# Kernel tuning notes

Measured on AMD Instinct MI355X. Metric: run time of the kernel, lower is better.

## Reference

```python
import jax, jax.numpy as jnp
import numpy as np
import math

B, S, D, H = 2, 2048, 2048, 16
DH = D // H  # 128


def _rope(x, cos, sin):
    # x: [b, s, h, dh]; cos/sin: [s, dh//2]
    b, s, h, dh = x.shape
    x2 = x.reshape(b, s, h, dh // 2, 2)
    a, bb = x2[..., 0], x2[..., 1]
    c = cos[None, :, None, :]
    sn = sin[None, :, None, :]
    out = jnp.stack([a * c - bb * sn, a * sn + bb * c], axis=-1)
    return out.reshape(b, s, h, dh)


def setup_inputs() -> dict:
    key = jax.random.key(0)
    ks = jax.random.split(key, 6)
    x = jax.random.normal(ks[0], (B, S, D), dtype=jnp.float32)
    # RoPE frequencies (theta=10000) as cos/sin of shape [S, DH//2]
    inv_freq = 1.0 / (10000.0 ** (np.arange(0, DH, 2, dtype=np.float32) / DH))
    t = np.arange(S, dtype=np.float32)
    ang = jnp.asarray(np.outer(t, inv_freq))  # [S, DH//2]
    freqs_cos = jnp.cos(ang)
    freqs_sin = jnp.sin(ang)
    # causal additive mask [1,1,S,S]
    neg = jnp.finfo(jnp.float32).min
    mask = jnp.where(jnp.tril(jnp.ones((S, S), dtype=bool)), 0.0, neg)[None, None]
    sc = 0.02
    wq = jax.random.normal(ks[1], (D, D), dtype=jnp.float32) * sc
    wk = jax.random.normal(ks[2], (D, D), dtype=jnp.float32) * sc
    wv = jax.random.normal(ks[3], (D, D), dtype=jnp.float32) * sc
    wo = jax.random.normal(ks[4], (D, D), dtype=jnp.float32) * sc
    return {"x": x, "freqs_cos": freqs_cos, "freqs_sin": freqs_sin,
            "mask": mask, "wq": wq, "wk": wk, "wv": wv, "wo": wo}


def reference(x, freqs_cos, freqs_sin, mask, wq, wk, wv, wo):
    b, s, _ = x.shape
    # torch Linear: y = x @ W.T (weights stored [out, in])
    xq = (x @ wq.T).reshape(b, s, H, DH)
    xk = (x @ wk.T).reshape(b, s, H, DH)
    xv = (x @ wv.T).reshape(b, s, H, DH)
    xq = _rope(xq, freqs_cos, freqs_sin)
    xk = _rope(xk, freqs_cos, freqs_sin)
    # [b, h, s, dh]
    q = xq.transpose(0, 2, 1, 3)
    k = xk.transpose(0, 2, 1, 3)
    v = xv.transpose(0, 2, 1, 3)
    scores = jnp.einsum('bhqd,bhkd->bhqk', q, k) / math.sqrt(DH)
    scores = scores + mask
    attn = jax.nn.softmax(scores, axis=-1)  # dropout p=0 (eval)
    out = jnp.einsum('bhqk,bhkd->bhqd', attn, v)
    out = out.transpose(0, 2, 1, 3).reshape(b, s, D)
    return out @ wo.T
```

## Files before the change

### kernel.cpp

```cpp
#include <hip/hip_runtime.h>

#define B_ 2
#define S_ 2048
#define D_ 2048
#define H_ 16
#define DH_ 128

typedef __bf16 bf16_8 __attribute__((ext_vector_type(8)));
typedef __bf16 bf16_4 __attribute__((ext_vector_type(4)));
typedef float f32x4 __attribute__((ext_vector_type(4)));

__device__ __forceinline__ f32x4 mfma16(bf16_8 a, bf16_8 b, f32x4 c) {
  return __builtin_amdgcn_mfma_f32_16x16x32_bf16(a, b, c, 0, 0, 0);
}

__device__ __forceinline__ bf16_8 load8(const float* p) {
  f32x4 a = *(const f32x4*)p;
  f32x4 b = *(const f32x4*)(p + 4);
  bf16_8 r;
  r[0] = (__bf16)a[0]; r[1] = (__bf16)a[1]; r[2] = (__bf16)a[2]; r[3] = (__bf16)a[3];
  r[4] = (__bf16)b[0]; r[5] = (__bf16)b[1]; r[6] = (__bf16)b[2]; r[7] = (__bf16)b[3];
  return r;
}

__device__ __forceinline__ void async16(const __bf16* g, __bf16* l) {
  __builtin_amdgcn_global_load_lds(
      (const __attribute__((address_space(1))) void*)g,
      (__attribute__((address_space(3))) void*)l, 16, 0, 0);
}

__global__ __launch_bounds__(256) void cvt_all(
    const float* __restrict__ x, const float* __restrict__ wq,
    const float* __restrict__ wk, const float* __restrict__ wv,
    const float* __restrict__ wo, __bf16* __restrict__ xb,
    __bf16* __restrict__ wqb, __bf16* __restrict__ wkb,
    __bf16* __restrict__ wvb, __bf16* __restrict__ wob)
{
  const int W8 = (D_ * D_) / 8;
  int i = blockIdx.x * 256 + threadIdx.x;
  if (i < 2 * W8) {
    *(bf16_8*)(xb + (size_t)i * 8) = load8(x + (size_t)i * 8);
  } else {
    int j = i - 2 * W8;
    int sel = j >> 19, off = j & (W8 - 1);
    const float* s = sel == 0 ? wq : sel == 1 ? wk : sel == 2 ? wv : wo;
    __bf16* d = sel == 0 ? wqb : sel == 1 ? wkb : sel == 2 ? wvb : wob;
    *(bf16_8*)(d + (size_t)off * 8) = load8(s + (size_t)off * 8);
  }
}

template <bool WB>
__global__ __launch_bounds__(256) void qkv_gemm(
    const __bf16* __restrict__ A,
    const float* __restrict__ wqf, const float* __restrict__ wkf,
    const float* __restrict__ wvf,
    const __bf16* __restrict__ wqb, const __bf16* __restrict__ wkb,
    const __bf16* __restrict__ wvb,
    const float* __restrict__ fc, const float* __restrict__ fs,
    __bf16* __restrict__ Qo, __bf16* __restrict__ Ko, __bf16* __restrict__ Vo)
{
  constexpr int TILE = 128 * 32;
  constexpr int STAGE_ELEMS = WB ? 4 * TILE : (128 * 32 + 128 * 40);
  constexpr int TS_ELEMS = 64 * 136;
  constexpr int SM_ELEMS = STAGE_ELEMS > TS_ELEMS ? STAGE_ELEMS : TS_ELEMS;
  __shared__ __align__(16) __bf16 smem[SM_ELEMS];

  const int tid = threadIdx.x;
  const int wave = tid >> 6, lane = tid & 63;
  const int quad = lane >> 4, l16 = lane & 15;
  const int m0 = blockIdx.y * 128, n0 = blockIdx.x * 128;
  const int wsel = n0 >> 11, nloc = n0 & 2047;
  const int wm = (wave >> 1) * 64, wn = (wave & 1) * 64;
  const __bf16* agl = A + (size_t)(m0 + wave * 32 + (lane >> 2)) * 2048 + (lane & 3) * 8;
  f32x4 acc[4][4] = {};
  if (WB) {
    const __bf16* Wb = wsel == 0 ? wqb : wsel == 1 ? wkb : wvb;
    const __bf16* wgl = Wb + (size_t)(nloc + wave * 32 + (lane >> 2)) * 2048 + (lane & 3) * 8;
    auto STAGE = [&](int k0, int p) {
      __bf16* ab = smem + p * TILE + (wave * 32) * 32;
      __bf16* wb2 = smem + 2 * TILE + p * TILE + (wave * 32) * 32;
      async16(agl + k0,             ab);
      async16(agl + 16 * 2048 + k0, ab + 16 * 32);
      async16(wgl + k0,             wb2);
      async16(wgl + 16 * 2048 + k0, wb2 + 16 * 32);
    };
    STAGE(0, 0);
#pragma unroll 2
    for (int it = 0; it < 64; ++it) {
      const int p = it & 1;
      if (it + 1 < 64) {
        STAGE((it + 1) * 32, p ^ 1);
        asm volatile("s_waitcnt vmcnt(4)" ::: "memory");
      } else {
        asm volatile("s_waitcnt vmcnt(0)" ::: "memory");
      }
      __builtin_amdgcn_s_barrier();
      asm volatile("" ::: "memory");
      const __bf16* Ab = smem + p * TILE;
      const __bf16* Wbuf = smem + 2 * TILE + p * TILE;
      bf16_8 af[4], bfr[4];
      for (int i = 0; i < 4; ++i) {
        af[i]  = *(const bf16_8*)(Ab   + (wm + i * 16 + l16) * 32 + quad * 8);
        bfr[i] = *(const bf16_8*)(Wbuf + (wn + i * 16 + l16) * 32 + quad * 8);
      }
      for (int mi = 0; mi < 4; ++mi)
        for (int ni = 0; ni < 4; ++ni)
          acc[mi][ni] = mfma16(af[mi], bfr[ni], acc[mi][ni]);
      asm volatile("s_waitcnt lgkmcnt(0)" ::: "memory");
      __builtin_amdgcn_s_barrier();
      asm volatile("" ::: "memory");
    }
  } else {
    auto As = (__bf16(*)[32])smem;
    auto Ws = (__bf16(*)[40])(smem + 128 * 32);
    const float* W = wsel == 0 ? wqf : wsel == 1 ? wkf : wvf;
    const int srow = tid >> 1, scol = (tid & 1) * 16;
    const float* wg = W + (size_t)(nloc + srow) * 2048 + scol;
    for (int k0 = 0; k0 < 2048; k0 += 32) {
      __syncthreads();
      async16(agl + k0,             &As[wave * 32][0]);
      async16(agl + 16 * 2048 + k0, &As[wave * 32 + 16][0]);
      *(bf16_8*)&Ws[srow][scol]     = load8(wg + k0);
      *(bf16_8*)&Ws[srow][scol + 8] = load8(wg + k0 + 8);
      __syncthreads();
      bf16_8 af[4], bfr[4];
      for (int i = 0; i < 4; ++i) {
        af[i]  = *(const bf16_8*)&As[wm + i * 16 + l16][quad * 8];
        bfr[i] = *(const bf16_8*)&Ws[wn + i * 16 + l16][quad * 8];
      }
      for (int mi = 0; mi < 4; ++mi)
        for (int ni = 0; ni < 4; ++ni)
          acc[mi][ni] = mfma16(af[mi], bfr[ni], acc[mi][ni]);
    }
  }
  if (wsel < 2) {
    const float qscale = wsel == 0 ? 0.08838834764831845f * 1.4426950408889634f
                                   : 1.0f;
    __bf16* O = wsel == 0 ? Qo : Ko;
    for (int mi = 0; mi < 4; ++mi)
      for (int ni = 0; ni < 4; ++ni)
        for (int r = 0; r < 4; ++r) {
          int row = m0 + wm + mi * 16 + quad * 4 + r;
          int col = nloc + wn + ni * 16 + l16;
          float self = acc[mi][ni][r];
          float oth = __shfl_xor(self, 1);
          int s = row & (S_ - 1);
          int dh = col & (DH_ - 1);
          float c = fc[s * (DH_ / 2) + (dh >> 1)];
          float sn = fs[s * (DH_ / 2) + (dh >> 1)];
          float o = (dh & 1) ? (oth * sn + self * c) : (self * c - oth * sn);
          O[(size_t)row * 2048 + col] = (__bf16)(o * qscale);
        }
  } else {
    auto Ts = (__bf16(*)[136])smem;
    const int b = m0 >> 11, h = nloc >> 7;
    __bf16* vb = Vo + ((size_t)(b * H_ + h) * DH_) * S_ + (m0 & (S_ - 1));
    for (int p = 0; p < 2; ++p) {
      __syncthreads();
      if ((wn >> 6) == p) {
        for (int mi = 0; mi < 4; ++mi)
          for (int ni = 0; ni < 4; ++ni) {
            int cl = ni * 16 + l16;
            int rl = wm + mi * 16 + quad * 4;
            bf16_4 pk;
            for (int r = 0; r < 4; ++r) pk[r] = (__bf16)acc[mi][ni][r];
            *(bf16_4*)&Ts[cl][rl] = pk;
          }
      }
      __syncthreads();
      for (int i = 0; i < 4; ++i) {
        int dh = p * 64 + i * 16 + (tid >> 4);
        int sc = (tid & 15) * 8;
        *(bf16_8*)(vb + (size_t)dh * S_ + sc) = *(const bf16_8*)&Ts[dh - p * 64][sc];
      }
    }
  }
}

template <bool WB>
__global__ __launch_bounds__(256) void out_gemm(
    const __bf16* __restrict__ A, const float* __restrict__ Wf,
    const __bf16* __restrict__ Wb, float* __restrict__ C)
{
  constexpr int TILE = 128 * 32;
  constexpr int SM_ELEMS = WB ? 4 * TILE : (128 * 32 + 128 * 40);
  __shared__ __align__(16) __bf16 smem[SM_ELEMS];
  const int tid = threadIdx.x;
  const int wave = tid >> 6, lane = tid & 63;
  const int quad = lane >> 4, l16 = lane & 15;
  const int m0 = blockIdx.y * 128, n0 = blockIdx.x * 128;
  const int wm = (wave >> 1) * 64, wn = (wave & 1) * 64;
  const __bf16* agl = A + (size_t)(m0 + wave * 32 + (lane >> 2)) * 2048 + (lane & 3) * 8;
  f32x4 acc[4][4] = {};
  if (WB) {
    const __bf16* wgl = Wb + (size_t)(n0 + wave * 32 + (lane >> 2)) * 2048 + (lane & 3) * 8;
    auto STAGE = [&](int k0, int p) {
      __bf16* ab = smem + p * TILE + (wave * 32) * 32;
      __bf16* wb2 = smem + 2 * TILE + p * TILE + (wave * 32) * 32;
      async16(agl + k0,             ab);
      async16(agl + 16 * 2048 + k0, ab + 16 * 32);
      async16(wgl + k0,             wb2);
      async16(wgl + 16 * 2048 + k0, wb2 + 16 * 32);
    };
    STAGE(0, 0);
#pragma unroll 2
    for (int it = 0; it < 64; ++it) {
      const int p = it & 1;
      if (it + 1 < 64) {
        STAGE((it + 1) * 32, p ^ 1);
        asm volatile("s_waitcnt vmcnt(4)" ::: "memory");
      } else {
        asm volatile("s_waitcnt vmcnt(0)" ::: "memory");
      }
      __builtin_amdgcn_s_barrier();
      asm volatile("" ::: "memory");
      const __bf16* Ab = smem + p * TILE;
      const __bf16* Wbuf = smem + 2 * TILE + p * TILE;
      bf16_8 af[4], bfr[4];
      for (int i = 0; i < 4; ++i) {
        af[i]  = *(const bf16_8*)(Ab   + (wm + i * 16 + l16) * 32 + quad * 8);
        bfr[i] = *(const bf16_8*)(Wbuf + (wn + i * 16 + l16) * 32 + quad * 8);
      }
      for (int mi = 0; mi < 4; ++mi)
        for (int ni = 0; ni < 4; ++ni)
          acc[mi][ni] = mfma16(af[mi], bfr[ni], acc[mi][ni]);
      asm volatile("s_waitcnt lgkmcnt(0)" ::: "memory");
      __builtin_amdgcn_s_barrier();
      asm volatile("" ::: "memory");
    }
  } else {
    auto As = (__bf16(*)[32])smem;
    auto Ws = (__bf16(*)[40])(smem + 128 * 32);
    const int srow = tid >> 1, scol = (tid & 1) * 16;
    const float* wg = Wf + (size_t)(n0 + srow) * 2048 + scol;
    for (int k0 = 0; k0 < 2048; k0 += 32) {
      __syncthreads();
      async16(agl + k0,             &As[wave * 32][0]);
      async16(agl + 16 * 2048 + k0, &As[wave * 32 + 16][0]);
      *(bf16_8*)&Ws[srow][scol]     = load8(wg + k0);
      *(bf16_8*)&Ws[srow][scol + 8] = load8(wg + k0 + 8);
      __syncthreads();
      bf16_8 af[4], bfr[4];
      for (int i = 0; i < 4; ++i) {
        af[i]  = *(const bf16_8*)&As[wm + i * 16 + l16][quad * 8];
        bfr[i] = *(const bf16_8*)&Ws[wn + i * 16 + l16][quad * 8];
      }
      for (int mi = 0; mi < 4; ++mi)
        for (int ni = 0; ni < 4; ++ni)
          acc[mi][ni] = mfma16(af[mi], bfr[ni], acc[mi][ni]);
    }
  }
  for (int mi = 0; mi < 4; ++mi)
    for (int ni = 0; ni < 4; ++ni)
      for (int r = 0; r < 4; ++r) {
        int row = m0 + wm + mi * 16 + quad * 4 + r;
        int col = n0 + wn + ni * 16 + l16;
        C[(size_t)row * 2048 + col] = acc[mi][ni][r];
      }
}

__global__ __launch_bounds__(256) void attn_kernel(
    const __bf16* __restrict__ Q, const __bf16* __restrict__ K,
    const __bf16* __restrict__ Vt_g, __bf16* __restrict__ O)
{
  __shared__ __bf16 Ks[2][64 * 128];
  __shared__ __bf16 Vt[128 * 64];
  __shared__ __bf16 Ps[4][32][72];
  const int tid = threadIdx.x;
  const int wave = tid >> 6, lane = tid & 63;
  const int quad = lane >> 4, l16 = lane & 15;
  const int fid = blockIdx.y * gridDim.x + blockIdx.x;
  const int tid_swz = (fid & 7) * 64 + (fid >> 3);
  const int bh = tid_swz >> 4;
  const int qt = 15 - (tid_swz & 15);
  const size_t base = (size_t)(bh >> 4) * S_ * D_ + (size_t)(bh & 15) * DH_;
  const size_t vtb = (size_t)bh * DH_ * S_;
  const int q0 = qt * 128;
  const int wmin = q0 + wave * 32;

  bf16_8 qf[2][4];
  for (int qs = 0; qs < 2; ++qs) {
    int qrow = wmin + qs * 16 + l16;
    for (int kk = 0; kk < 4; ++kk)
      qf[qs][kk] = *(const bf16_8*)(Q + base + (size_t)qrow * D_ + kk * 32 + quad * 8);
  }
  asm volatile("s_waitcnt vmcnt(0)" ::: "memory");

  const int krs = wave * 4 + (lane >> 4);
  const __bf16* kgl = K + base + (size_t)krs * D_ + ((lane & 15) ^ krs) * 8;
  const int vrs = wave * 8 + (lane >> 3);
  const __bf16* vgl = Vt_g + vtb + (size_t)vrs * S_ + ((lane & 7) ^ (lane >> 3)) * 8;

  f32x4 oacc[2][8] = {};
  float lsum[2][4] = {};
  const int nt = 2 * qt + 2;

  for (int p = 0; p < 4; ++p)
    async16(kgl + (size_t)(p * 16) * D_, Ks[0] + (p * 16 + wave * 4) * 128);
  for (int p = 0; p < 4; ++p)
    async16(vgl + (size_t)(p * 32) * S_, Vt + (p * 32 + wave * 8) * 64);

  int cur = 0;
  for (int kt = 0; kt < nt; ++kt) {
    const bool more = (kt + 1 < nt);
    if (more) {
      for (int p = 0; p < 4; ++p)
        async16(kgl + (size_t)((kt + 1) * 64 + p * 16) * D_,
                Ks[cur ^ 1] + (p * 16 + wave * 4) * 128);
      asm volatile("s_waitcnt vmcnt(8)" ::: "memory");
    } else {
      asm volatile("s_waitcnt vmcnt(4)" ::: "memory");
    }
    __builtin_amdgcn_s_barrier();
    asm volatile("" ::: "memory");

    const bool active = (kt * 64 <= wmin + 31);
    if (active) {
      const bool diag = (kt * 64 + 63 > wmin);
      const __bf16* ksb = Ks[cur];
      for (int n = 0; n < 4; ++n) {
        f32x4 s0 = {}, s1 = {};
        __builtin_amdgcn_s_setprio(1);
#pragma unroll
        for (int kk = 0; kk < 4; ++kk) {
          bf16_8 kf = *(const bf16_8*)&ksb[(n * 16 + l16) * 128 + (((kk * 4 + quad) ^ l16) * 8)];
          s0 = mfma16(qf[0][kk], kf, s0);
          s1 = mfma16(qf[1][kk], kf, s1);
        }
        __builtin_amdgcn_s_setprio(0);
#pragma unroll
        for (int qs = 0; qs < 2; ++qs) {
          f32x4 sv = qs ? s1 : s0;
          for (int r = 0; r < 4; ++r) {
            float v = sv[r];
            if (diag) {
              int qr = wmin + qs * 16 + quad * 4 + r;
              if (kt * 64 + n * 16 + l16 > qr) v = -INFINITY;
            }
            float p = exp2f(v);
            lsum[qs][r] += p;
            Ps[wave][qs * 16 + quad * 4 + r][n * 16 + l16] = (__bf16)p;
          }
        }
      }
    }

    if (more) asm volatile("s_waitcnt vmcnt(4)" ::: "memory");
    else      asm volatile("s_waitcnt vmcnt(0)" ::: "memory");
    __builtin_amdgcn_s_barrier();
    asm volatile("" ::: "memory");

    if (active) {
      bf16_8 pf0[2], pf1[2];
      for (int qs = 0; qs < 2; ++qs) {
        pf0[qs] = *(const bf16_8*)&Ps[wave][qs * 16 + l16][quad * 8];
        pf1[qs] = *(const bf16_8*)&Ps[wave][qs * 16 + l16][32 + quad * 8];
      }
      __builtin_amdgcn_s_setprio(1);
#pragma unroll
      for (int nc = 0; nc < 8; ++nc) {
        bf16_8 vf0 = *(const bf16_8*)&Vt[(nc * 16 + l16) * 64 + ((quad ^ (l16 & 7)) * 8)];
        bf16_8 vf1 = *(const bf16_8*)&Vt[(nc * 16 + l16) * 64 + (((quad + 4) ^ (l16 & 7)) * 8)];
        oacc[0][nc] = mfma16(pf0[0], vf0, oacc[0][nc]);
        oacc[0][nc] = mfma16(pf1[0], vf1, oacc[0][nc]);
        oacc[1][nc] = mfma16(pf0[1], vf0, oacc[1][nc]);
        oacc[1][nc] = mfma16(pf1[1], vf1, oacc[1][nc]);
      }
      __builtin_amdgcn_s_setprio(0);
    }

    asm volatile("s_waitcnt lgkmcnt(0)" ::: "memory");
    __builtin_amdgcn_s_barrier();
    asm volatile("" ::: "memory");
    if (more)
      for (int p = 0; p < 4; ++p)
        async16(vgl + (size_t)(p * 32) * S_ + (size_t)(kt + 1) * 64,
                Vt + (p * 32 + wave * 8) * 64);
    cur ^= 1;
  }

  for (int qs = 0; qs < 2; ++qs)
    for (int r = 0; r < 4; ++r) {
      float l = lsum[qs][r];
      l += __shfl_xor(l, 1);
      l += __shfl_xor(l, 2);
      l += __shfl_xor(l, 4);
      l += __shfl_xor(l, 8);
      float rinv = 1.f / l;
      int qr = wmin + qs * 16 + quad * 4 + r;
      for (int nc = 0; nc < 8; ++nc)
        O[base + (size_t)qr * D_ + nc * 16 + l16] = (__bf16)(oacc[qs][nc][r] * rinv);
    }
}

extern "C" void kernel_launch(void* const* d_in, const int* in_sizes, int n_in,
                              void* d_out, int out_size, void* d_ws, size_t ws_size,
                              hipStream_t stream)
{
  const float* x    = (const float*)d_in[0];
  const float* fcos = (const float*)d_in[1];
  const float* fsin = (const float*)d_in[2];
  const float* wq   = (const float*)d_in[4];
  const float* wk   = (const float*)d_in[5];
  const float* wv   = (const float*)d_in[6];
  const float* wo   = (const float*)d_in[7];
  float* out = (float*)d_out;

  const size_t T = (size_t)B_ * S_ * D_;
  const size_t W = (size_t)D_ * D_;
  __bf16* xb  = (__bf16*)d_ws;
  __bf16* qw  = xb + T;
  __bf16* kw  = qw + T;
  __bf16* vt  = kw + T;
  __bf16* wqb = vt + T;
  __bf16* wkb = wqb + W;
  __bf16* wvb = wkb + W;
  __bf16* wob = wvb + W;
  __bf16* ow  = xb;

  const bool wb = ws_size >= (4 * T + 4 * W) * sizeof(__bf16);
  const int W8 = (int)(W / 8);
  cvt_all<<<(wb ? 6 : 2) * W8 / 256, 256, 0, stream>>>(
      x, wq, wk, wv, wo, xb, wqb, wkb, wvb, wob);
  if (wb)
    qkv_gemm<true><<<dim3(48, 32), 256, 0, stream>>>(
        xb, nullptr, nullptr, nullptr, wqb, wkb, wvb, fcos, fsin, qw, kw, vt);
  else
    qkv_gemm<false><<<dim3(48, 32), 256, 0, stream>>>(
        xb, wq, wk, wv, nullptr, nullptr, nullptr, fcos, fsin, qw, kw, vt);
  attn_kernel<<<dim3(S_ / 128, B_ * H_), 256, 0, stream>>>(qw, kw, vt, ow);
  if (wb)
    out_gemm<true><<<dim3(16, 32), 256, 0, stream>>>(ow, nullptr, wob, out);
  else
    out_gemm<false><<<dim3(16, 32), 256, 0, stream>>>(ow, wo, nullptr, out);
}
```

Baseline: 427.6 us.

## Add 256x256-tile 8-wave QKV GEMM with swizzled LDS and phased pipelining

Replaces the 128x128-tile QKV projection GEMM with a new kernel that uses 256x256 output tiles, 512 threads (8 waves), and a 64-wide K step. Tiles are double-buffered in 128 KB of LDS with an XOR-swizzled layout, and each K step is split into four sub-quadrant phases that interleave async global loads with MFMA work and raise wave priority around the math. The larger tiles are meant to cut global memory traffic per FLOP and hide load latency. The costs are higher register and LDS pressure and a grid of only 384 blocks, which may underfill the GPU. The RoPE, scaling and V-transpose epilogues are reimplemented for the new tile shape.

```diff
diff --git a/kernel.cpp b/kernel.cpp
--- a/kernel.cpp
+++ b/kernel.cpp
@@ -49,6 +49,162 @@
   }
 }
 
+template <int QA, int QB, typename STG, typename WT>
+__device__ __forceinline__ void phase8(
+    const __bf16* Ab, const __bf16* Bb, int wsm64, int wsn32, int l16,
+    int colx0, int colx1, f32x4 (&acc)[4][4][2], STG&& stg, WT&& wt)
+{
+  bf16_8 af[4][2], bfr[2][2];
+#pragma unroll
+  for (int mi = 0; mi < 4; ++mi) {
+    const __bf16* ap = Ab + (QA * 128 + wsm64 + mi * 16 + l16) * 64;
+    af[mi][0] = *(const bf16_8*)(ap + colx0);
+    af[mi][1] = *(const bf16_8*)(ap + colx1);
+  }
+#pragma unroll
+  for (int ni = 0; ni < 2; ++ni) {
+    const __bf16* bp = Bb + (QB * 128 + wsn32 + ni * 16 + l16) * 64;
+    bfr[ni][0] = *(const bf16_8*)(bp + colx0);
+    bfr[ni][1] = *(const bf16_8*)(bp + colx1);
+  }
+  stg();
+  wt();
+  __builtin_amdgcn_s_barrier();
+  asm volatile("s_waitcnt lgkmcnt(0)" ::: "memory");
+  __builtin_amdgcn_s_setprio(1);
+#pragma unroll
+  for (int mi = 0; mi < 4; ++mi)
+#pragma unroll
+    for (int ni = 0; ni < 2; ++ni) {
+      acc[QA * 2 + QB][mi][ni] = mfma16(af[mi][0], bfr[ni][0], acc[QA * 2 + QB][mi][ni]);
+      acc[QA * 2 + QB][mi][ni] = mfma16(af[mi][1], bfr[ni][1], acc[QA * 2 + QB][mi][ni]);
+    }
+  __builtin_amdgcn_s_setprio(0);
+  asm volatile("" ::: "memory");
+  __builtin_amdgcn_s_barrier();
+  asm volatile("" ::: "memory");
+}
+
+__global__ __launch_bounds__(512, 2) void qkv_gemm8(
+    const __bf16* __restrict__ A,
+    const __bf16* __restrict__ wqb, const __bf16* __restrict__ wkb,
+    const __bf16* __restrict__ wvb,
+    const float* __restrict__ fc, const float* __restrict__ fs,
+    __bf16* __restrict__ Qo, __bf16* __restrict__ Ko, __bf16* __restrict__ Vo)
+{
+  __shared__ __align__(16) __bf16 smem8[65536];
+  const int tid = threadIdx.x;
+  const int wave = tid >> 6, lane = tid & 63;
+  const int quad = lane >> 4, l16 = lane & 15;
+  const int wsm64 = (wave & 1) * 64;
+  const int wsn32 = (wave >> 1) * 32;
+  const int m0 = blockIdx.y * 256, n0 = blockIdx.x * 256;
+  const int wsel = n0 >> 11, nloc = n0 & 2047;
+  const __bf16* Wb = wsel == 0 ? wqb : wsel == 1 ? wkb : wvb;
+
+  const int srow = wave * 8 + (lane >> 3);
+  const int scol = ((lane & 7) ^ (lane >> 3)) * 8;
+  const __bf16* agl = A  + (size_t)(m0 + srow) * 2048 + scol;
+  const __bf16* wgl = Wb + (size_t)(nloc + srow) * 2048 + scol;
+  const int ldso = wave * 8 * 64;
+
+  const int colx0 = (quad * 8) ^ ((l16 & 7) * 8);
+  const int colx1 = colx0 ^ 32;
+
+  f32x4 acc[4][4][2] = {};
+
+  auto SA8 = [&](int kt, int h, int q) {
+    async16(agl + (size_t)(h * 128 + q * 64) * 2048 + (size_t)kt * 64,
+            smem8 + (kt & 1) * 16384 + (h * 128 + q * 64) * 64 + ldso);
+  };
+  auto SB8 = [&](int kt, int h, int q) {
+    async16(wgl + (size_t)(h * 128 + q * 64) * 2048 + (size_t)kt * 64,
+            smem8 + 32768 + (kt & 1) * 16384 + (h * 128 + q * 64) * 64 + ldso);
+  };
+
+  SA8(0, 0, 0); SA8(0, 0, 1); SB8(0, 0, 0); SB8(0, 0, 1);
+  SA8(0, 1, 0); SA8(0, 1, 1); SB8(0, 1, 0); SB8(0, 1, 1);
+  SA8(1, 0, 0); SA8(1, 0, 1); SB8(1, 0, 0); SB8(1, 0, 1);
+  asm volatile("s_waitcnt vmcnt(4)" ::: "memory");
+  __builtin_amdgcn_s_barrier();
+  asm volatile("" ::: "memory");
+
+  const int nG = 2048 / 64;
+  for (int g = 0; g < nG; ++g) {
+    const __bf16* Ab = smem8 + (g & 1) * 16384;
+    const __bf16* Bb = smem8 + 32768 + (g & 1) * 16384;
+    phase8<0, 0>(Ab, Bb, wsm64, wsn32, l16, colx0, colx1, acc,
+        [&] { if (g + 1 < nG) { SA8(g + 1, 1, 0); SA8(g + 1, 1, 1); } },
+        [&] { if (g == nG - 1) asm volatile("s_waitcnt vmcnt(0)" ::: "memory"); });
+    phase8<0, 1>(Ab, Bb, wsm64, wsn32, l16, colx0, colx1, acc,
+        [&] { if (g + 1 < nG) { SB8(g + 1, 1, 0); SB8(g + 1, 1, 1); } },
+        [&] {});
+    phase8<1, 0>(Ab, Bb, wsm64, wsn32, l16, colx0, colx1, acc,
+        [&] { if (g + 2 < nG) { SA8(g + 2, 0, 0); SA8(g + 2, 0, 1); } },
+        [&] {});
+    phase8<1, 1>(Ab, Bb, wsm64, wsn32, l16, colx0, colx1, acc,
+        [&] { if (g + 2 < nG) { SB8(g + 2, 0, 0); SB8(g + 2, 0, 1); } },
+        [&] { asm volatile("s_waitcnt vmcnt(4)" ::: "memory"); });
+  }
+
+  if (wsel < 2) {
+    const float qscale = wsel == 0 ? 0.08838834764831845f * 1.4426950408889634f
+                                   : 1.0f;
+    __bf16* O = wsel == 0 ? Qo : Ko;
+#pragma unroll
+    for (int q = 0; q < 4; ++q)
+#pragma unroll
+      for (int mi = 0; mi < 4; ++mi)
+#pragma unroll
+        for (int ni = 0; ni < 2; ++ni)
+#pragma unroll
+          for (int r = 0; r < 4; ++r) {
+            int row = m0 + (q >> 1) * 128 + wsm64 + mi * 16 + quad * 4 + r;
+            int col = nloc + (q & 1) * 128 + wsn32 + ni * 16 + l16;
+            float self = acc[q][mi][ni][r];
+            float oth = __shfl_xor(self, 1);
+            int s = row & (S_ - 1);
+            int dh = col & (DH_ - 1);
+            float c = fc[s * (DH_ / 2) + (dh >> 1)];
+            float sn = fs[s * (DH_ / 2) + (dh >> 1)];
+            float o = (dh & 1) ? (oth * sn + self * c) : (self * c - oth * sn);
+            O[(size_t)row * 2048 + col] = (__bf16)(o * qscale);
+          }
+  } else {
+    auto Ts = (__bf16(*)[264])smem8;
+    const int b = m0 >> 11, sb = m0 & (S_ - 1);
+#pragma unroll
+    for (int p = 0; p < 4; ++p) {
+      __syncthreads();
+      if ((wsn32 >> 6) == (p & 1)) {
+        const int qb = p >> 1;
+#pragma unroll
+        for (int qa = 0; qa < 2; ++qa)
+#pragma unroll
+          for (int mi = 0; mi < 4; ++mi)
+#pragma unroll
+            for (int ni = 0; ni < 2; ++ni) {
+              int cl = (wsn32 & 32) + ni * 16 + l16;
+              int rl = qa * 128 + wsm64 + mi * 16 + quad * 4;
+              bf16_4 pk;
+#pragma unroll
+              for (int r = 0; r < 4; ++r) pk[r] = (__bf16)acc[qa * 2 + qb][mi][ni][r];
+              *(bf16_4*)&Ts[cl][rl] = pk;
+            }
+      }
+      __syncthreads();
+      const int h = (nloc + p * 64) >> 7, dh0 = (nloc + p * 64) & (DH_ - 1);
+      __bf16* vb = Vo + ((size_t)(b * H_ + h) * DH_ + dh0) * S_ + sb;
+#pragma unroll
+      for (int i = 0; i < 4; ++i) {
+        int dhl = i * 16 + (tid >> 5);
+        int sc = (tid & 31) * 8;
+        *(bf16_8*)(vb + (size_t)dhl * S_ + sc) = *(const bf16_8*)&Ts[dhl][sc];
+      }
+    }
+  }
+}
+
 template <bool WB>
 __global__ __launch_bounds__(256) void qkv_gemm(
     const __bf16* __restrict__ A,
@@ -74,8 +230,8 @@
   const __bf16* agl = A + (size_t)(m0 + wave * 32 + (lane >> 2)) * 2048 + (lane & 3) * 8;
   f32x4 acc[4][4] = {};
   if (WB) {
-    const __bf16* Wb = wsel == 0 ? wqb : wsel == 1 ? wkb : wvb;
-    const __bf16* wgl = Wb + (size_t)(nloc + wave * 32 + (lane >> 2)) * 2048 + (lane & 3) * 8;
+    const __bf16* Wbp = wsel == 0 ? wqb : wsel == 1 ? wkb : wvb;
+    const __bf16* wgl = Wbp + (size_t)(nloc + wave * 32 + (lane >> 2)) * 2048 + (lane & 3) * 8;
     auto STAGE = [&](int k0, int p) {
       __bf16* ab = smem + p * TILE + (wave * 32) * 32;
       __bf16* wb2 = smem + 2 * TILE + p * TILE + (wave * 32) * 32;
@@ -423,8 +579,8 @@
   cvt_all<<<(wb ? 6 : 2) * W8 / 256, 256, 0, stream>>>(
       x, wq, wk, wv, wo, xb, wqb, wkb, wvb, wob);
   if (wb)
-    qkv_gemm<true><<<dim3(48, 32), 256, 0, stream>>>(
-        xb, nullptr, nullptr, nullptr, wqb, wkb, wvb, fcos, fsin, qw, kw, vt);
+    qkv_gemm8<<<dim3(24, 16), 512, 0, stream>>>(
+        xb, wqb, wkb, wvb, fcos, fsin, qw, kw, vt);
   else
     qkv_gemm<false><<<dim3(48, 32), 256, 0, stream>>>(
         xb, wq, wk, wv, nullptr, nullptr, nullptr, fcos, fsin, qw, kw, vt);
```

After: 429.4 us. About the same (+0.4%).
